# Kernel tuning notes

Hardware: AMD Instinct MI355X
Metric: run time of the kernel (lower is better)

## Reference

```python
import jax, jax.numpy as jnp
import numpy as np

B, S, D = 2, 2048, 2048
H, HD = 16, 128          # num_heads, head_dim (H*HD == D)
I = 4096                 # intermediate_size; ffn in-dim is 2*I
EPS = 1e-5


def rmsnorm(x, w):
    return x * jax.lax.rsqrt(jnp.mean(x * x, axis=-1, keepdims=True) + EPS) * w


def setup_inputs() -> dict:
    key = jax.random.key(0)
    ks = jax.random.split(key, 12)
    sd = 0.02
    return {
        "hidden_states": jax.random.normal(ks[0], (B, S, D), jnp.float32),
        "attention_mask": jnp.zeros((B, S), jnp.float32),  # additive mask
        "rn1_w": jnp.ones((D,), jnp.float32),
        "wq": jax.random.normal(ks[1], (D, D), jnp.float32) * sd,
        "wk": jax.random.normal(ks[2], (D, D), jnp.float32) * sd,
        "wv": jax.random.normal(ks[3], (D, D), jnp.float32) * sd,
        "wo": jax.random.normal(ks[4], (D, D), jnp.float32) * sd,
        "rn2_w": jnp.ones((D,), jnp.float32),
        "w1": jax.random.normal(ks[5], (D, 2 * I), jnp.float32) * sd,      # Linear(d, 2*I, bias=False)
        "fc1_w": jax.random.normal(ks[6], (2 * I, I), jnp.float32) * sd,   # SwiGLU fc1
        "fc1_b": jnp.zeros((I,), jnp.float32),
        "fc2_w": jax.random.normal(ks[7], (2 * I, I), jnp.float32) * sd,   # SwiGLU fc2
        "fc2_b": jnp.zeros((I,), jnp.float32),
        "w3": jax.random.normal(ks[8], (I, D), jnp.float32) * sd,          # Linear(I, d, bias=False)
    }


def reference(hidden_states, attention_mask, rn1_w, wq, wk, wv, wo, rn2_w,
              w1, fc1_w, fc1_b, fc2_w, fc2_b, w3):
    # --- attention ---
    attn_in = rmsnorm(hidden_states, rn1_w)
    q = (attn_in @ wq).reshape(B, S, H, HD)
    k = (attn_in @ wk).reshape(B, S, H, HD)
    v = (attn_in @ wv).reshape(B, S, H, HD)
    # rope_cache is None -> no rotary embedding applied
    scores = jnp.einsum("bqhd,bkhd->bhqk", q, k) / np.sqrt(HD).astype(np.float32)
    scores = scores + attention_mask[:, None, None, :]  # [B,1,1,S] broadcast
    probs = jax.nn.softmax(scores, axis=-1)             # dropout p=0 (eval)
    attn = jnp.einsum("bhqk,bkhd->bqhd", probs, v).reshape(B, S, D)
    residual1 = hidden_states + attn @ wo
    # --- SwiGLU FFN ---
    ffn_in = rmsnorm(residual1, rn2_w)
    x = ffn_in @ w1                                      # [B,S,2I]
    gated = jax.nn.silu(x @ fc1_w + fc1_b) * (x @ fc2_w + fc2_b)  # [B,S,I]
    return residual1 + gated @ w3
```

## Files before the change

### kernel.cpp

```cpp
#include <hip/hip_runtime.h>
#include <hip/hip_bf16.h>
#include <stdint.h>

using short8 = __attribute__((ext_vector_type(8))) short;
using uint4v = __attribute__((ext_vector_type(4))) unsigned int;
using f32x4  = __attribute__((ext_vector_type(4))) float;

#define DEV __device__ __forceinline__

DEV float b2f(unsigned short u) {
  union { unsigned int i; float f; } v; v.i = ((unsigned int)u) << 16; return v.f;
}
DEV unsigned short f2b(float f) {
  union { float f; unsigned int i; } v; v.f = f;
  unsigned int x = v.i;
  return (unsigned short)((x + 0x7FFFu + ((x >> 16) & 1u)) >> 16);
}
DEV void g2lds16(const void* g, void* l) {
  __builtin_amdgcn_global_load_lds((const __attribute__((address_space(1))) void*)g,
                                   (__attribute__((address_space(3))) void*)l, 16, 0, 0);
}

DEV void xcd_rect_map(int wg, int nbx, int rby, int rbx, int& by, int& bx) {
  const int xcd_cols = nbx / rbx;
  const int xcd = wg & 7, local = wg >> 3;
  const int xr = xcd / xcd_cols, xc = xcd % xcd_cols;
  by = xr * rby + local / rbx;
  bx = xc * rbx + local % rbx;
}

enum { EPI_BF16 = 0, EPI_RESID_F32 = 1, EPI_BIAS_BF16 = 2, EPI_RESID_OUT = 3, EPI_SWIGLU = 4 };

template<int EPI>
__global__ __launch_bounds__(512, 2)
void gemm_bt256(const unsigned short* __restrict__ A, const unsigned short* __restrict__ Bt,
                void* __restrict__ Cout, const void* __restrict__ extra,
                const void* __restrict__ extra2, int M, int N, int K, int rby, int rbx) {
  __shared__ __align__(16) unsigned short As[2][256 * 64];
  __shared__ __align__(16) unsigned short Bs3[3][256 * 64];
  int by, bx;
  xcd_rect_map(blockIdx.x, N >> 8, rby, rbx, by, bx);
  const int m0 = by << 8, n0 = bx << 8;
  const int t = threadIdx.x;
  const int l = t & 63, wid = t >> 6;
  const int lr = l & 15, lg = l >> 4;
  const int wr = (wid >> 2) << 7;
  const int wc = (wid & 3) << 6;

  f32x4 acc[8][4];
#pragma unroll
  for (int i = 0; i < 8; ++i)
#pragma unroll
    for (int j = 0; j < 4; ++j) acc[i][j] = (f32x4){0.f, 0.f, 0.f, 0.f};

  const int sr = t >> 3;
  const int scSwz = ((t & 7) << 3) ^ ((sr & 7) << 3);
  const unsigned short* Ag = A  + (size_t)(m0 + sr) * K + scSwz;
  const unsigned short* Bg = Bt + (size_t)(n0 + sr) * K + scSwz;
  const int nT = K >> 6;

  const unsigned short* AgNext = Ag + 64;
  const unsigned short* BgNext2 = Bg + 128;
  const size_t rowK64 = (size_t)64 * K;

  const int xorv = (lr & 7) << 3;
  const int cb0 = (lg * 8) ^ xorv;
  const int cb1 = (32 + lg * 8) ^ xorv;

  short8 afA[2][2], afB[2][2], bfrA[4][2], bfrB[4][2];

#define STAGE_A(buf)                                                  \
  {                                                                   \
    unsigned short* dst = &As[buf][t * 8];                            \
    _Pragma("unroll")                                                 \
    for (int ld = 0; ld < 4; ++ld)                                    \
      g2lds16(AgNext + (size_t)ld * rowK64, dst + ld * 4096);         \
  }
#define STAGE_B2(slot)                                                \
  {                                                                   \
    unsigned short* dst = &Bs3[slot][t * 8];                          \
    _Pragma("unroll")                                                 \
    for (int ld = 0; ld < 4; ++ld)                                    \
      g2lds16(BgNext2 + (size_t)ld * rowK64, dst + ld * 4096);        \
  }
#define READ_A(dst, base, p)                                          \
  {                                                                   \
    const int ro0 = (wr + ((p) * 2 + 0) * 16 + lr) << 6;              \
    const int ro1 = (wr + ((p) * 2 + 1) * 16 + lr) << 6;              \
    dst[0][0] = *(const short8*)((base) + ro0 + cb0);                 \
    dst[0][1] = *(const short8*)((base) + ro0 + cb1);                 \
    dst[1][0] = *(const short8*)((base) + ro1 + cb0);                 \
    dst[1][1] = *(const short8*)((base) + ro1 + cb1);                 \
  }
#define READ_B(dst, base)                                             \
  {                                                                   \
    _Pragma("unroll")                                                 \
    for (int ni = 0; ni < 4; ++ni) {                                  \
      const int ro = (wc + ni * 16 + lr) << 6;                        \
      dst[ni][0] = *(const short8*)((base) + ro + cb0);               \
      dst[ni][1] = *(const short8*)((base) + ro + cb1);               \
    }                                                                 \
  }
#define MFMA_PH(af, bfr, r0)                                          \
  {                                                                   \
    _Pragma("unroll")                                                 \
    for (int kk = 0; kk < 2; ++kk)                                    \
      _Pragma("unroll")                                               \
      for (int a = 0; a < 2; ++a)                                     \
        _Pragma("unroll")                                             \
        for (int ni = 0; ni < 4; ++ni)                                \
          acc[(r0) + a][ni] = __builtin_amdgcn_mfma_f32_16x16x32_bf16(\
              af[a][kk], bfr[ni][kk], acc[(r0) + a][ni], 0, 0, 0);    \
  }

#define TILE_BODY(tt, BFR, BFRN)                                      \
  {                                                                   \
    const unsigned short* baseA = &As[(tt) & 1][0];                   \
    const bool more1 = ((tt) + 1) < nT;                               \
    const bool more2 = ((tt) + 2) < nT;                               \
    READ_A(afB, baseA, 1);                                            \
    if (more1) STAGE_A(((tt) + 1) & 1);                               \
    asm volatile("s_waitcnt lgkmcnt(4)" ::: "memory");                \
    __builtin_amdgcn_sched_barrier(0);                                \
    __builtin_amdgcn_s_setprio(1);                                    \
    MFMA_PH(afA, BFR, 0);                                             \
    __builtin_amdgcn_s_setprio(0);                                    \
    READ_A(afA, baseA, 2);                                            \
    if (more2) STAGE_B2(bs2);                                         \
    asm volatile("s_waitcnt lgkmcnt(4)" ::: "memory");                \
    __builtin_amdgcn_sched_barrier(0);                                \
    __builtin_amdgcn_s_setprio(1);                                    \
    MFMA_PH(afB, BFR, 2);                                             \
    __builtin_amdgcn_s_setprio(0);                                    \
    READ_A(afB, baseA, 3);                                            \
    if (more1) {                                                      \
      if (more2) asm volatile("s_waitcnt vmcnt(8)" ::: "memory");     \
      else       asm volatile("s_waitcnt vmcnt(4)" ::: "memory");     \
    }                                                                 \
    asm volatile("s_waitcnt lgkmcnt(4)" ::: "memory");                \
    __builtin_amdgcn_sched_barrier(0);                                \
    __builtin_amdgcn_s_setprio(1);                                    \
    MFMA_PH(afA, BFR, 4);                                             \
    __builtin_amdgcn_s_setprio(0);                                    \
    if (more1) {                                                      \
      READ_B(BFRN, &Bs3[bnext][0]);                                   \
      asm volatile("s_waitcnt lgkmcnt(8)" ::: "memory");              \
    } else {                                                          \
      asm volatile("s_waitcnt lgkmcnt(0)" ::: "memory");              \
    }                                                                 \
    __builtin_amdgcn_sched_barrier(0);                                \
    __builtin_amdgcn_s_setprio(1);                                    \
    MFMA_PH(afB, BFR, 6);                                             \
    __builtin_amdgcn_s_setprio(0);                                    \
    if (more1) {                                                      \
      if (more2) asm volatile("s_waitcnt vmcnt(4)" ::: "memory");     \
      else       asm volatile("s_waitcnt vmcnt(0)" ::: "memory");     \
      asm volatile("s_barrier" ::: "memory");                         \
      AgNext += 64;                                                   \
      BgNext2 += 64;                                                  \
      bnext = (bnext == 2) ? 0 : bnext + 1;                           \
      bs2  = (bs2 == 2) ? 0 : bs2 + 1;                                \
      READ_A(afA, &As[((tt) + 1) & 1][0], 0);                         \
    }                                                                 \
  }

  {
    unsigned short* dstA = &As[0][t * 8];
    unsigned short* dstB = &Bs3[0][t * 8];
#pragma unroll
    for (int ld = 0; ld < 4; ++ld) {
      g2lds16(Ag + (size_t)ld * rowK64, dstA + ld * 4096);
      g2lds16(Bg + (size_t)ld * rowK64, dstB + ld * 4096);
    }
  }
  {
    unsigned short* dstB1 = &Bs3[1][t * 8];
    const unsigned short* srcB1 = Bg + 64;
#pragma unroll
    for (int ld = 0; ld < 4; ++ld) g2lds16(srcB1 + (size_t)ld * rowK64, dstB1 + ld * 4096);
  }
  asm volatile("s_waitcnt vmcnt(4)\n\ts_barrier" ::: "memory");

  int bnext = 1;
  int bs2 = 2;
  READ_A(afA, &As[0][0], 0);
  READ_B(bfrA, &Bs3[0][0]);

  for (int tp = 0; tp < nT; tp += 2) {
    TILE_BODY(tp,     bfrA, bfrB);
    TILE_BODY(tp + 1, bfrB, bfrA);
  }
#undef STAGE_A
#undef STAGE_B2
#undef READ_A
#undef READ_B
#undef MFMA_PH
#undef TILE_BODY

#pragma unroll
  for (int mi = 0; mi < 8; ++mi) {
#pragma unroll
    for (int ni = 0; ni < 4; ++ni) {
      const int col = n0 + wc + ni * 16 + lr;
#pragma unroll
      for (int j = 0; j < 4; ++j) {
        const int row = m0 + wr + mi * 16 + lg * 4 + j;
        const size_t idx = (size_t)row * N + col;
        const float v = acc[mi][ni][j];
        if constexpr (EPI == EPI_BF16) {
          ((unsigned short*)Cout)[idx] = f2b(v);
        } else if constexpr (EPI == EPI_RESID_F32) {
          ((float*)Cout)[idx] = v + ((const float*)extra)[idx];
        } else if constexpr (EPI == EPI_BIAS_BF16) {
          ((unsigned short*)Cout)[idx] = f2b(v + ((const float*)extra)[col]);
        } else if constexpr (EPI == EPI_SWIGLU) {
          const float g1v = b2f(((const unsigned short*)extra2)[idx]);
          const float v2 = v + ((const float*)extra)[col];
          ((unsigned short*)Cout)[idx] = f2b(g1v / (1.f + __expf(-g1v)) * v2);
        } else {
          ((float*)Cout)[idx] = v + ((const float*)extra)[idx];
        }
      }
    }
  }
}

template<int EPI>
__global__ __launch_bounds__(256)
void gemm_bt(const unsigned short* __restrict__ A, const unsigned short* __restrict__ Bt,
             void* __restrict__ Cout, const void* __restrict__ extra,
             int M, int N, int K, int rby, int rbx) {
  __shared__ __align__(16) unsigned short As[2][128 * 64];
  __shared__ __align__(16) unsigned short Bs[2][128 * 64];
  int by, bx;
  xcd_rect_map(blockIdx.x, N >> 7, rby, rbx, by, bx);
  const int m0 = by << 7, n0 = bx << 7;
  const int t = threadIdx.x;
  const int l = t & 63, w = t >> 6;
  const int lr = l & 15, lg = l >> 4;
  const int wr = (w >> 1) << 6, wc = (w & 1) << 6;

  f32x4 acc[4][4];
#pragma unroll
  for (int i = 0; i < 4; ++i)
#pragma unroll
    for (int j = 0; j < 4; ++j) acc[i][j] = (f32x4){0.f, 0.f, 0.f, 0.f};

  const int sr = t >> 3;
  const int skSwz = ((t & 7) << 3) ^ ((sr & 7) << 3);
  const unsigned short* Ag = A  + (size_t)(m0 + sr) * K + skSwz;
  const unsigned short* Bg = Bt + (size_t)(n0 + sr) * K + skSwz;
  const int nT = K >> 6;

  const int xorv2 = (lr & 7) << 3;
  const int c0s = (lg * 8) ^ xorv2;
  const int c1s = (32 + lg * 8) ^ xorv2;

  {
    unsigned short* dstA = &As[0][t * 8];
    unsigned short* dstB = &Bs[0][t * 8];
#pragma unroll
    for (int c = 0; c < 4; ++c) {
      g2lds16(Ag + (size_t)(c * 32) * K, dstA + c * 2048);
      g2lds16(Bg + (size_t)(c * 32) * K, dstB + c * 2048);
    }
  }
  asm volatile("s_waitcnt vmcnt(0)\n\ts_barrier" ::: "memory");

  for (int tt = 0; tt < nT; ++tt) {
    const int cur = tt & 1;
    const bool more = (tt + 1) < nT;
    if (more) {
      unsigned short* dstA = &As[cur ^ 1][t * 8];
      unsigned short* dstB = &Bs[cur ^ 1][t * 8];
      const unsigned short* sA = Ag + ((size_t)(tt + 1) << 6);
      const unsigned short* sB = Bg + ((size_t)(tt + 1) << 6);
#pragma unroll
      for (int c = 0; c < 4; ++c) {
        g2lds16(sA + (size_t)(c * 32) * K, dstA + c * 2048);
        g2lds16(sB + (size_t)(c * 32) * K, dstB + c * 2048);
      }
    }
    const unsigned short* Ab = &As[cur][0];
    const unsigned short* Bb = &Bs[cur][0];
    short8 af[2][4], bfr[2][4];
#pragma unroll
    for (int mi = 0; mi < 4; ++mi) {
      const int ro = (wr + mi * 16 + lr) << 6;
      af[0][mi] = *(const short8*)(Ab + ro + c0s);
      af[1][mi] = *(const short8*)(Ab + ro + c1s);
    }
#pragma unroll
    for (int ni = 0; ni < 4; ++ni) {
      const int ro = (wc + ni * 16 + lr) << 6;
      bfr[0][ni] = *(const short8*)(Bb + ro + c0s);
      bfr[1][ni] = *(const short8*)(Bb + ro + c1s);
    }
    asm volatile("s_waitcnt lgkmcnt(0)" ::: "memory");
    __builtin_amdgcn_sched_barrier(0);
    __builtin_amdgcn_s_setprio(1);
#pragma unroll
    for (int ks = 0; ks < 2; ++ks)
#pragma unroll
      for (int mi = 0; mi < 4; ++mi)
#pragma unroll
        for (int ni = 0; ni < 4; ++ni)
          acc[mi][ni] = __builtin_amdgcn_mfma_f32_16x16x32_bf16(af[ks][mi], bfr[ks][ni], acc[mi][ni], 0, 0, 0);
    __builtin_amdgcn_s_setprio(0);
    asm volatile("s_waitcnt vmcnt(0)\n\ts_barrier" ::: "memory");
  }

#pragma unroll
  for (int mi = 0; mi < 4; ++mi) {
#pragma unroll
    for (int ni = 0; ni < 4; ++ni) {
      const int col = n0 + wc + ni * 16 + lr;
#pragma unroll
      for (int j = 0; j < 4; ++j) {
        const int row = m0 + wr + mi * 16 + lg * 4 + j;
        const size_t idx = (size_t)row * N + col;
        const float v = acc[mi][ni][j];
        if constexpr (EPI == EPI_BF16) {
          ((unsigned short*)Cout)[idx] = f2b(v);
        } else if constexpr (EPI == EPI_RESID_F32) {
          ((float*)Cout)[idx] = v + ((const float*)extra)[idx];
        } else if constexpr (EPI == EPI_BIAS_BF16) {
          ((unsigned short*)Cout)[idx] = f2b(v + ((const float*)extra)[col]);
        } else {
          ((float*)Cout)[idx] = v + ((const float*)extra)[idx];
        }
      }
    }
  }
}

__global__ __launch_bounds__(256)
void attn_fwd(const unsigned short* __restrict__ qkv, const unsigned short* __restrict__ vt,
              const float* __restrict__ mask, unsigned short* __restrict__ out) {
  __shared__ __align__(16) unsigned short Vs[128 * 64];
  __shared__ __align__(16) unsigned short Ps[4][16 * 64];
  const int b = blockIdx.z, hh = blockIdx.y;
  const int q0 = blockIdx.x << 6;
  const int t = threadIdx.x, l = t & 63, w = t >> 6;
  const int lr = l & 15, lg = l >> 4;
  const float scale = 0.08838834764831845f;

  short8 qf[4];
  {
    const unsigned short* qb = qkv + (size_t)(b * 2048 + q0 + w * 16 + lr) * 6144 + hh * 128;
#pragma unroll
    for (int ks = 0; ks < 4; ++ks) qf[ks] = *(const short8*)(qb + ks * 32 + lg * 8);
  }
  f32x4 acc_o[8];
#pragma unroll
  for (int i = 0; i < 8; ++i) acc_o[i] = (f32x4){0.f, 0.f, 0.f, 0.f};
  float m_r[4], l_r[4];
#pragma unroll
  for (int j = 0; j < 4; ++j) { m_r[j] = -1e30f; l_r[j] = 0.f; }

  const unsigned short* kb = qkv + (size_t)(b * 2048) * 6144 + 2048 + hh * 128;
  const unsigned short* vb = vt + (size_t)(b * 16 + hh) * 128 * 2048;
  const float* mb = mask + b * 2048;

  for (int kt = 0; kt < 2048; kt += 64) {
#pragma unroll
    for (int c = 0; c < 4; ++c) {
      const int e = (c * 256 + t) * 8;
      const int vr = e >> 6, vc = e & 63;
      g2lds16(vb + (size_t)vr * 2048 + kt + (vc ^ ((vr & 7) << 3)), Vs + e);
    }
    __syncthreads();

    f32x4 sc[4];
    __builtin_amdgcn_s_setprio(1);
#pragma unroll
    for (int nt = 0; nt < 4; ++nt) {
      f32x4 s = (f32x4){0.f, 0.f, 0.f, 0.f};
      const unsigned short* krow = kb + (size_t)(kt + nt * 16 + lr) * 6144 + lg * 8;
#pragma unroll
      for (int ks = 0; ks < 4; ++ks) {
        short8 kf = *(const short8*)(krow + ks * 32);
        s = __builtin_amdgcn_mfma_f32_16x16x32_bf16(qf[ks], kf, s, 0, 0, 0);
      }
      sc[nt] = s;
    }
    __builtin_amdgcn_s_setprio(0);
#pragma unroll
    for (int nt = 0; nt < 4; ++nt) {
      const float mv = mb[kt + nt * 16 + lr];
#pragma unroll
      for (int j = 0; j < 4; ++j) sc[nt][j] = sc[nt][j] * scale + mv;
    }
#pragma unroll
    for (int j = 0; j < 4; ++j) {
      float tm = fmaxf(fmaxf(sc[0][j], sc[1][j]), fmaxf(sc[2][j], sc[3][j]));
      tm = fmaxf(tm, __shfl_xor(tm, 1));
      tm = fmaxf(tm, __shfl_xor(tm, 2));
      tm = fmaxf(tm, __shfl_xor(tm, 4));
      tm = fmaxf(tm, __shfl_xor(tm, 8));
      const bool skip = __all(tm - m_r[j] <= 8.f);
      float corr = 1.f;
      float mn = m_r[j];
      if (!skip) {
        mn = fmaxf(m_r[j], tm);
        corr = __expf(m_r[j] - mn);
        m_r[j] = mn;
      }
      float ps = 0.f;
#pragma unroll
      for (int nt = 0; nt < 4; ++nt) {
        const float p = __expf(sc[nt][j] - mn);
        sc[nt][j] = p;
        ps += p;
      }
      ps += __shfl_xor(ps, 1);
      ps += __shfl_xor(ps, 2);
      ps += __shfl_xor(ps, 4);
      ps += __shfl_xor(ps, 8);
      l_r[j] = l_r[j] * corr + ps;
      if (!skip) {
#pragma unroll
        for (int di = 0; di < 8; ++di) acc_o[di][j] *= corr;
      }
    }
#pragma unroll
    for (int nt = 0; nt < 4; ++nt)
#pragma unroll
      for (int j = 0; j < 4; ++j) {
        const int q = lg * 4 + j;
        Ps[w][(q << 6) + ((nt * 16 + lr) ^ ((q & 7) << 3))] = f2b(sc[nt][j]);
      }
    asm volatile("s_waitcnt lgkmcnt(0)" ::: "memory");
    __builtin_amdgcn_s_setprio(1);
#pragma unroll
    for (int ks2 = 0; ks2 < 2; ++ks2) {
      short8 pf = *(const short8*)(&Ps[w][(lr << 6) + ((ks2 * 32 + lg * 8) ^ ((lr & 7) << 3))]);
#pragma unroll
      for (int di = 0; di < 8; ++di) {
        short8 vf = *(const short8*)(Vs + ((di * 16 + lr) << 6) + ((ks2 * 32 + lg * 8) ^ ((lr & 7) << 3)));
        acc_o[di] = __builtin_amdgcn_mfma_f32_16x16x32_bf16(pf, vf, acc_o[di], 0, 0, 0);
      }
    }
    __builtin_amdgcn_s_setprio(0);
    __syncthreads();
  }
#pragma unroll
  for (int di = 0; di < 8; ++di)
#pragma unroll
    for (int j = 0; j < 4; ++j) {
      const int q = q0 + w * 16 + lg * 4 + j;
      out[(size_t)(b * 2048 + q) * 2048 + hh * 128 + di * 16 + lr] = f2b(acc_o[di][j] / l_r[j]);
    }
}

__global__ __launch_bounds__(256)
void rmsnorm_k(const float* __restrict__ in, const float* __restrict__ wgt,
               unsigned short* __restrict__ out) {
  __shared__ float red[4];
  const int row = blockIdx.x, t = threadIdx.x;
  const float4* rp = (const float4*)(in + (size_t)row * 2048 + t * 8);
  float4 a = rp[0], b = rp[1];
  float x[8] = {a.x, a.y, a.z, a.w, b.x, b.y, b.z, b.w};
  float s = 0.f;
#pragma unroll
  for (int i = 0; i < 8; ++i) s += x[i] * x[i];
#pragma unroll
  for (int m = 1; m < 64; m <<= 1) s += __shfl_xor(s, m);
  const int l = t & 63, w = t >> 6;
  if (l == 0) red[w] = s;
  __syncthreads();
  const float tot = red[0] + red[1] + red[2] + red[3];
  const float rr = rsqrtf(tot * (1.f / 2048.f) + 1e-5f);
  const float4* wp = (const float4*)(wgt + t * 8);
  float4 wa = wp[0], wb = wp[1];
  float ww[8] = {wa.x, wa.y, wa.z, wa.w, wb.x, wb.y, wb.z, wb.w};
  short8 o;
#pragma unroll
  for (int i = 0; i < 8; ++i) o[i] = (short)f2b(x[i] * rr * ww[i]);
  *(short8*)(out + (size_t)row * 2048 + t * 8) = o;
}

__global__ __launch_bounds__(256)
void transpose2d(const float* __restrict__ in, unsigned short* __restrict__ out,
                 int R, int C) {
  __shared__ __align__(16) unsigned int tile2[64][36];
  const int r0 = blockIdx.y << 6, c0 = blockIdx.x << 6;
  const int t = threadIdx.x;
#pragma unroll
  for (int it = 0; it < 2; ++it) {
    const int p = it * 256 + t;
    const int r2 = p >> 4;
    const int c = (p & 15) << 2;
    const float* src = in + (size_t)(r0 + r2 * 2) * C + c0 + c;
    float4 va = *(const float4*)(src);
    float4 vb = *(const float4*)(src + C);
    tile2[c + 0][r2] = (unsigned int)f2b(va.x) | ((unsigned int)f2b(vb.x) << 16);
    tile2[c + 1][r2] = (unsigned int)f2b(va.y) | ((unsigned int)f2b(vb.y) << 16);
    tile2[c + 2][r2] = (unsigned int)f2b(va.z) | ((unsigned int)f2b(vb.z) << 16);
    tile2[c + 3][r2] = (unsigned int)f2b(va.w) | ((unsigned int)f2b(vb.w) << 16);
  }
  __syncthreads();
#pragma unroll
  for (int it = 0; it < 2; ++it) {
    const int u = it * 256 + t;
    const int rr = u >> 3;
    const int k8 = u & 7;
    uint4v v = *(const uint4v*)(&tile2[rr][k8 * 4]);
    short8 o;
#pragma unroll
    for (int j = 0; j < 4; ++j) {
      o[2 * j]     = (short)(v[j] & 0xFFFFu);
      o[2 * j + 1] = (short)(v[j] >> 16);
    }
    *(short8*)(out + (size_t)(c0 + rr) * R + r0 + k8 * 8) = o;
  }
}

__global__ __launch_bounds__(256)
void transpose_v(const unsigned short* __restrict__ qkv, unsigned short* __restrict__ vt) {
  __shared__ __align__(16) unsigned short tile[64][72];
  const int s0 = blockIdx.x << 6, d0 = blockIdx.y << 6;
  const int z = blockIdx.z;
  const unsigned short* in = qkv + (size_t)((z >> 4) * 2048) * 6144 + 4096 + (z & 15) * 128;
  unsigned short* outp = vt + (size_t)z * 128 * 2048;
  const int t = threadIdx.x;
#pragma unroll
  for (int it = 0; it < 2; ++it) {
    const int e = (it * 256 + t) * 8;
    const int r = e >> 6, cc = e & 63;
    short8 v = *(const short8*)(in + (size_t)(s0 + r) * 6144 + d0 + cc);
#pragma unroll
    for (int i = 0; i < 8; ++i) tile[cc + i][r] = (unsigned short)v[i];
  }
  __syncthreads();
#pragma unroll
  for (int it = 0; it < 2; ++it) {
    const int e = (it * 256 + t) * 8;
    const int rr = e >> 6, kk = e & 63;
    short8 v = *(const short8*)(&tile[rr][kk]);
    *(short8*)(outp + (size_t)(d0 + rr) * 2048 + s0 + kk) = v;
  }
}

extern "C" void kernel_launch(void* const* d_in, const int* in_sizes, int n_in,
                              void* d_out, int out_size, void* d_ws, size_t ws_size,
                              hipStream_t stream) {
  const float* h    = (const float*)d_in[0];
  const float* mask = (const float*)d_in[1];
  const float* rn1w = (const float*)d_in[2];
  const float* wq   = (const float*)d_in[3];
  const float* wk   = (const float*)d_in[4];
  const float* wv   = (const float*)d_in[5];
  const float* wo   = (const float*)d_in[6];
  const float* rn2w = (const float*)d_in[7];
  const float* w1   = (const float*)d_in[8];
  const float* fc1w = (const float*)d_in[9];
  const float* fc1b = (const float*)d_in[10];
  const float* fc2w = (const float*)d_in[11];
  const float* fc2b = (const float*)d_in[12];
  const float* w3   = (const float*)d_in[13];

  char* ws = (char*)d_ws;
  size_t off = 0;
  auto alloc = [&](size_t bytes) { char* p = ws + off; off += (bytes + 255) & ~(size_t)255; return p; };
  unsigned short* bufA = (unsigned short*)alloc(16777216);
  unsigned short* bufB = (unsigned short*)alloc(16777216);
  unsigned short* qkv  = (unsigned short*)alloc(50331648);
  float*          r1f  = (float*)alloc(33554432);
  unsigned short* xbuf = (unsigned short*)alloc(67108864);
  unsigned short* g1   = (unsigned short*)alloc(33554432);
  unsigned short* wt   = (unsigned short*)alloc(67108864);
  if (off > ws_size) return;

  rmsnorm_k<<<4096, 256, 0, stream>>>(h, rn1w, bufA);
  transpose2d<<<dim3(32, 32), 256, 0, stream>>>(wq, wt,                 2048, 2048);
  transpose2d<<<dim3(32, 32), 256, 0, stream>>>(wk, wt + 2048 * 2048,   2048, 2048);
  transpose2d<<<dim3(32, 32), 256, 0, stream>>>(wv, wt + 2 * 2048 * 2048, 2048, 2048);
  gemm_bt256<EPI_BF16><<<384, 512, 0, stream>>>(bufA, wt, qkv, nullptr, nullptr, 4096, 6144, 2048, 8, 6);
  transpose_v<<<dim3(32, 2, 32), 256, 0, stream>>>(qkv, bufB);
  attn_fwd<<<dim3(32, 16, 2), 256, 0, stream>>>(qkv, bufB, mask, bufA);
  transpose2d<<<dim3(32, 32), 256, 0, stream>>>(wo, wt, 2048, 2048);
  gemm_bt<EPI_RESID_F32><<<512, 256, 0, stream>>>(bufA, wt, r1f, h, 4096, 2048, 2048, 8, 8);

  rmsnorm_k<<<4096, 256, 0, stream>>>(r1f, rn2w, bufB);
  transpose2d<<<dim3(128, 32), 256, 0, stream>>>(w1, wt, 2048, 8192);
  gemm_bt256<EPI_BF16><<<512, 512, 0, stream>>>(bufB, wt, xbuf, nullptr, nullptr, 4096, 8192, 2048, 8, 8);
  transpose2d<<<dim3(64, 128), 256, 0, stream>>>(fc1w, wt, 8192, 4096);
  gemm_bt256<EPI_BIAS_BF16><<<256, 512, 0, stream>>>(xbuf, wt, g1, fc1b, nullptr, 4096, 4096, 8192, 4, 8);
  transpose2d<<<dim3(64, 128), 256, 0, stream>>>(fc2w, wt, 8192, 4096);
  unsigned short* gated = qkv;
  gemm_bt256<EPI_SWIGLU><<<256, 512, 0, stream>>>(xbuf, wt, gated, fc2b, g1, 4096, 4096, 8192, 4, 8);
  transpose2d<<<dim3(32, 64), 256, 0, stream>>>(w3, wt, 4096, 2048);
  gemm_bt<EPI_RESID_OUT><<<512, 256, 0, stream>>>(gated, wt, d_out, r1f, 4096, 2048, 4096, 8, 8);
}
```

Baseline: 1.309 ms.

## Double-buffer K and V tiles in LDS for attention and merge QKV weight transposes

The attention kernel now stages both K and V tiles into LDS through async global-to-LDS loads. It uses two buffers, so the next tile's load overlaps with the current tile's MFMA work, where before K was read straight from global memory inside the QK loop. LDS use grows from about 24 KB to 72 KB per block, which may reduce occupancy. Separately, the three Q/K/V weight transposes are fused into one launch with a z-dimension to cut launch overhead.

```diff
diff --git a/kernel.cpp b/kernel.cpp
--- a/kernel.cpp
+++ b/kernel.cpp
@@ -337,7 +337,8 @@
 __global__ __launch_bounds__(256)
 void attn_fwd(const unsigned short* __restrict__ qkv, const unsigned short* __restrict__ vt,
               const float* __restrict__ mask, unsigned short* __restrict__ out) {
-  __shared__ __align__(16) unsigned short Vs[128 * 64];
+  __shared__ __align__(16) unsigned short Ks[2][64 * 128];
+  __shared__ __align__(16) unsigned short Vs[2][128 * 64];
   __shared__ __align__(16) unsigned short Ps[4][16 * 64];
   const int b = blockIdx.z, hh = blockIdx.y;
   const int q0 = blockIdx.x << 6;
@@ -362,24 +363,36 @@
   const unsigned short* vb = vt + (size_t)(b * 16 + hh) * 128 * 2048;
   const float* mb = mask + b * 2048;
 
+#define STAGE_KV(buf, ktv)                                            \
+  {                                                                   \
+    _Pragma("unroll")                                                 \
+    for (int c = 0; c < 4; ++c) {                                     \
+      const int e = (c * 256 + t) * 8;                                \
+      const int kr = e >> 7, kc = e & 127;                            \
+      g2lds16(kb + (size_t)((ktv) + kr) * 6144 + (kc ^ ((kr & 7) << 3)), &Ks[buf][0] + e); \
+      const int vr = e >> 6, vc = e & 63;                             \
+      g2lds16(vb + (size_t)vr * 2048 + (ktv) + (vc ^ ((vr & 7) << 3)), &Vs[buf][0] + e);   \
+    }                                                                 \
+  }
+
+  STAGE_KV(0, 0);
+  asm volatile("s_waitcnt vmcnt(0)\n\ts_barrier" ::: "memory");
+
   for (int kt = 0; kt < 2048; kt += 64) {
-#pragma unroll
-    for (int c = 0; c < 4; ++c) {
-      const int e = (c * 256 + t) * 8;
-      const int vr = e >> 6, vc = e & 63;
-      g2lds16(vb + (size_t)vr * 2048 + kt + (vc ^ ((vr & 7) << 3)), Vs + e);
-    }
-    __syncthreads();
+    const int cur = (kt >> 6) & 1;
+    const bool more = (kt + 64) < 2048;
+    if (more) STAGE_KV(cur ^ 1, kt + 64);
+    const unsigned short* Kb = &Ks[cur][0];
+    const unsigned short* Vb = &Vs[cur][0];
 
     f32x4 sc[4];
     __builtin_amdgcn_s_setprio(1);
 #pragma unroll
     for (int nt = 0; nt < 4; ++nt) {
       f32x4 s = (f32x4){0.f, 0.f, 0.f, 0.f};
-      const unsigned short* krow = kb + (size_t)(kt + nt * 16 + lr) * 6144 + lg * 8;
 #pragma unroll
       for (int ks = 0; ks < 4; ++ks) {
-        short8 kf = *(const short8*)(krow + ks * 32);
+        short8 kf = *(const short8*)(Kb + ((nt * 16 + lr) << 7) + ((ks * 32 + lg * 8) ^ ((lr & 7) << 3)));
         s = __builtin_amdgcn_mfma_f32_16x16x32_bf16(qf[ks], kf, s, 0, 0, 0);
       }
       sc[nt] = s;
@@ -437,13 +450,14 @@
       short8 pf = *(const short8*)(&Ps[w][(lr << 6) + ((ks2 * 32 + lg * 8) ^ ((lr & 7) << 3))]);
 #pragma unroll
       for (int di = 0; di < 8; ++di) {
-        short8 vf = *(const short8*)(Vs + ((di * 16 + lr) << 6) + ((ks2 * 32 + lg * 8) ^ ((lr & 7) << 3)));
+        short8 vf = *(const short8*)(Vb + ((di * 16 + lr) << 6) + ((ks2 * 32 + lg * 8) ^ ((lr & 7) << 3)));
         acc_o[di] = __builtin_amdgcn_mfma_f32_16x16x32_bf16(pf, vf, acc_o[di], 0, 0, 0);
       }
     }
     __builtin_amdgcn_s_setprio(0);
-    __syncthreads();
-  }
+    asm volatile("s_waitcnt vmcnt(0)\n\ts_barrier" ::: "memory");
+  }
+#undef STAGE_KV
 #pragma unroll
   for (int di = 0; di < 8; ++di)
 #pragma unroll
@@ -513,6 +527,45 @@
       o[2 * j + 1] = (short)(v[j] >> 16);
     }
     *(short8*)(out + (size_t)(c0 + rr) * R + r0 + k8 * 8) = o;
+  }
+}
+
+__global__ __launch_bounds__(256)
+void transpose_qkvw(const float* __restrict__ wq, const float* __restrict__ wk,
+                    const float* __restrict__ wv, unsigned short* __restrict__ out) {
+  __shared__ __align__(16) unsigned int tile2[64][36];
+  const int z = blockIdx.z;
+  const float* in = (z == 0) ? wq : (z == 1) ? wk : wv;
+  unsigned short* outp = out + (size_t)z * 2048 * 2048;
+  const int r0 = blockIdx.y << 6, c0 = blockIdx.x << 6;
+  const int t = threadIdx.x;
+#pragma unroll
+  for (int it = 0; it < 2; ++it) {
+    const int p = it * 256 + t;
+    const int r2 = p >> 4;
+    const int c = (p & 15) << 2;
+    const float* src = in + (size_t)(r0 + r2 * 2) * 2048 + c0 + c;
+    float4 va = *(const float4*)(src);
+    float4 vb = *(const float4*)(src + 2048);
+    tile2[c + 0][r2] = (unsigned int)f2b(va.x) | ((unsigned int)f2b(vb.x) << 16);
+    tile2[c + 1][r2] = (unsigned int)f2b(va.y) | ((unsigned int)f2b(vb.y) << 16);
+    tile2[c + 2][r2] = (unsigned int)f2b(va.z) | ((unsigned int)f2b(vb.z) << 16);
+    tile2[c + 3][r2] = (unsigned int)f2b(va.w) | ((unsigned int)f2b(vb.w) << 16);
+  }
+  __syncthreads();
+#pragma unroll
+  for (int it = 0; it < 2; ++it) {
+    const int u = it * 256 + t;
+    const int rr = u >> 3;
+    const int k8 = u & 7;
+    uint4v v = *(const uint4v*)(&tile2[rr][k8 * 4]);
+    short8 o;
+#pragma unroll
+    for (int j = 0; j < 4; ++j) {
+      o[2 * j]     = (short)(v[j] & 0xFFFFu);
+      o[2 * j + 1] = (short)(v[j] >> 16);
+    }
+    *(short8*)(outp + (size_t)(c0 + rr) * 2048 + r0 + k8 * 8) = o;
   }
 }
 
@@ -573,9 +626,7 @@
   if (off > ws_size) return;
 
   rmsnorm_k<<<4096, 256, 0, stream>>>(h, rn1w, bufA);
-  transpose2d<<<dim3(32, 32), 256, 0, stream>>>(wq, wt,                 2048, 2048);
-  transpose2d<<<dim3(32, 32), 256, 0, stream>>>(wk, wt + 2048 * 2048,   2048, 2048);
-  transpose2d<<<dim3(32, 32), 256, 0, stream>>>(wv, wt + 2 * 2048 * 2048, 2048, 2048);
+  transpose_qkvw<<<dim3(32, 32, 3), 256, 0, stream>>>(wq, wk, wv, wt);
   gemm_bt256<EPI_BF16><<<384, 512, 0, stream>>>(bufA, wt, qkv, nullptr, nullptr, 4096, 6144, 2048, 8, 6);
   transpose_v<<<dim3(32, 2, 32), 256, 0, stream>>>(qkv, bufB);
   attn_fwd<<<dim3(32, 16, 2), 256, 0, stream>>>(qkv, bufB, mask, bufA);
```

After: 1.152 ms. 12.0% less time.
